# Performance work log

Hardware: AMD Instinct MI355X
Metric: run time of the kernel (lower is better)

## Reference

```python
import jax, jax.numpy as jnp
import numpy as np
from jax import lax

H = 16          # heads
K1, K2 = 3, 3   # kernel_size
LN_EPS = 1e-5


def _ln(x, g, b):
    m = jnp.mean(x, axis=-1, keepdims=True)
    v = jnp.mean(jnp.square(x - m), axis=-1, keepdims=True)
    return (x - m) * lax.rsqrt(v + LN_EPS) * g + b


def _gelu(x):
    return jax.nn.gelu(x, approximate=False)  # torch nn.GELU default (erf)


def setup_inputs() -> dict:
    key = jax.random.key(0)
    B, T, D, Th = 4, 1024, 1024, 256
    C = 2 * D  # context_dim
    ks = jax.random.split(key, 16)

    def w(k, shape):
        fan_in = shape[0]
        return (jax.random.normal(k, shape, jnp.float32) / np.sqrt(fan_in)).astype(jnp.float32)

    inp = {
        'x': jax.random.normal(ks[0], (B, T, D), jnp.float32),
        'historical_data': jax.random.normal(ks[1], (B, Th, D), jnp.float32),
        'Wq': w(ks[2], (D, D)),
        'Wk': w(ks[3], (D, D)),
        'Wv': w(ks[4], (D, D)),
        'hist_W': w(ks[5], (D, C)), 'hist_b': jnp.zeros((C,), jnp.float32),
        'hist_ln_g': jnp.ones((C,), jnp.float32), 'hist_ln_b': jnp.zeros((C,), jnp.float32),
        'ctx_W1': w(ks[6], (C, C // 4)), 'ctx_b1': jnp.zeros((C // 4,), jnp.float32),
        'ctx_W2': w(ks[7], (C // 4, 1)), 'ctx_b2': jnp.zeros((1,), jnp.float32),
        'kg_W1': w(ks[8], (C, D)), 'kg_b1': jnp.zeros((D,), jnp.float32),
        'kg_ln_g': jnp.ones((D,), jnp.float32), 'kg_ln_b': jnp.zeros((D,), jnp.float32),
        'kg_W2': w(ks[9], (D, H * K1 * K2)), 'kg_b2': jnp.zeros((H * K1 * K2,), jnp.float32),
        'proj_W': w(ks[10], (D, D)), 'proj_b': jnp.zeros((D,), jnp.float32),
        'causal_mask': jnp.triu(jnp.ones((T, T), bool), k=1),  # True = masked
    }
    return inp


def reference(x, historical_data, Wq, Wk, Wv, hist_W, hist_b, hist_ln_g, hist_ln_b,
              ctx_W1, ctx_b1, ctx_W2, ctx_b2, kg_W1, kg_b1, kg_ln_g, kg_ln_b,
              kg_W2, kg_b2, proj_W, proj_b, causal_mask):
    B, T, D = x.shape
    hd = D // H
    scale = hd ** -0.5

    # qkv projections (no bias), split heads -> [B, H, T, hd]
    q = (x @ Wq).reshape(B, T, H, hd).transpose(0, 2, 1, 3)
    k = (x @ Wk).reshape(B, T, H, hd).transpose(0, 2, 1, 3)
    v = (x @ Wv).reshape(B, T, H, hd).transpose(0, 2, 1, 3)

    attn = jnp.einsum('bhqd,bhkd->bhqk', q, k) * scale  # [B,H,T,T]

    # --- causal context from history ---
    eh = _gelu(_ln(historical_data @ hist_W + hist_b, hist_ln_g, hist_ln_b))  # [B,Th,C]
    aw = _gelu(eh @ ctx_W1 + ctx_b1) @ ctx_W2 + ctx_b2                        # [B,Th,1]
    aw = jax.nn.softmax(aw, axis=1)
    cc = jnp.sum(eh * aw, axis=1)                                             # [B,C]

    # --- per-(batch,head) 3x3 kernels ---
    kp = _gelu(_ln(cc @ kg_W1 + kg_b1, kg_ln_g, kg_ln_b)) @ kg_W2 + kg_b2     # [B,H*9]
    kernels = jax.nn.softmax(kp.reshape(B, H, K1 * K2), axis=-1)
    kernels = kernels.reshape(B * H, 1, K1, K2)

    # zero masked scores, then mix neighbors via grouped conv2d (cross-correlation)
    mask = causal_mask[None, None]  # [1,1,T,T]
    attn0 = jnp.where(mask, 0.0, attn).reshape(1, B * H, T, T)
    attn = lax.conv_general_dilated(
        attn0, kernels, window_strides=(1, 1),
        padding=((K1 // 2, K1 // 2), (K2 // 2, K2 // 2)),
        feature_group_count=B * H,
        dimension_numbers=('NCHW', 'OIHW', 'NCHW'),
    ).reshape(B, H, T, T)

    attn = jnp.where(mask, -jnp.inf, attn)
    p = jax.nn.softmax(attn, axis=-1)
    out = jnp.einsum('bhqk,bhkd->bhqd', p, v)           # [B,H,T,hd]
    out = out.transpose(0, 2, 1, 3).reshape(B, T, D)
    return out @ proj_W + proj_b
```

## Files before the change

kernel.cpp:

```cpp
#include <hip/hip_runtime.h>
#include <hip/hip_bf16.h>
#include <math.h>

#define DEV static __device__ __forceinline__

typedef __attribute__((ext_vector_type(4))) float f32x4;
typedef __attribute__((ext_vector_type(8))) __bf16 bf16x8;
typedef __attribute__((ext_vector_type(8))) short s16x8;
typedef __attribute__((ext_vector_type(2))) _Float16 h16x2;

DEV float b2f(short v){ unsigned u = ((unsigned)(unsigned short)v) << 16; float f; __builtin_memcpy(&f, &u, 4); return f; }
DEV short f2b(float f){ unsigned u; __builtin_memcpy(&u, &f, 4); unsigned r = (u + 0x7fffu + ((u >> 16) & 1u)) >> 16; return (short)r; }
DEV short f2h(float f){ _Float16 h = (_Float16)f; short s; __builtin_memcpy(&s, &h, 2); return s; }
DEV h16x2 u2h2(unsigned u){ h16x2 h; __builtin_memcpy(&h, &u, 4); return h; }
DEV float gelu_f(float v){ return 0.5f * v * (1.0f + erff(v * 0.70710678118654752f)); }

DEV void gload16(const void* g, void* l) {
  __builtin_amdgcn_global_load_lds((const __attribute__((address_space(1))) unsigned int*)g,
                                   (__attribute__((address_space(3))) unsigned int*)l, 16, 0, 0);
}

DEV void xy_swz(int& bx, int& by, int nx, int ny) {
  int lin = by * nx + bx;
  int q = (nx * ny) >> 3;
  int l2 = (lin & 7) * q + (lin >> 3);
  bx = l2 % nx; by = l2 / nx;
}

__global__ __launch_bounds__(256) void k_cast_all(const float* __restrict__ x, const float* __restrict__ hist,
                                                  short* __restrict__ xb, short* __restrict__ histb,
                                                  short* __restrict__ q, short* __restrict__ kk){
  int bid = blockIdx.x;
  if (bid >= 2560) {
    int idx = (bid - 2560) * 256 + threadIdx.x;
    int bh = idx >> 5, c = idx & 31;
    int which = c >> 3, chunk = c & 7;
    short* base = (which < 2) ? q : kk;
    size_t off = (size_t)bh * 1026 * 64 + ((which & 1) ? (size_t)1025 * 64 : 0) + chunk * 8;
    s16x8 zz = {};
    *(s16x8*)&base[off] = zz;
    return;
  }
  const float* in; short* out; int i;
  if (bid < 2048) { in = x; out = xb; i = (bid * 256 + threadIdx.x) * 8; }
  else            { in = hist; out = histb; i = ((bid - 2048) * 256 + threadIdx.x) * 8; }
  f32x4 a = *(const f32x4*)&in[i];
  f32x4 b = *(const f32x4*)&in[i + 4];
  s16x8 o;
  o[0]=f2b(a[0]); o[1]=f2b(a[1]); o[2]=f2b(a[2]); o[3]=f2b(a[3]);
  o[4]=f2b(b[0]); o[5]=f2b(b[1]); o[6]=f2b(b[2]); o[7]=f2b(b[3]);
  *(s16x8*)&out[i] = o;
}

DEV void tcast_tile(const float* __restrict__ W, short* __restrict__ Wt, int K, int N, int tx, int ty){
  __shared__ float tile[32][33];
  int nb = tx * 32, kb = ty * 32;
  int tid = threadIdx.x;
  int c = tid & 31, r0 = tid >> 5;
  #pragma unroll
  for (int r = r0; r < 32; r += 8) tile[r][c] = W[(size_t)(kb + r) * N + nb + c];
  __syncthreads();
  #pragma unroll
  for (int r = r0; r < 32; r += 8) Wt[(size_t)(nb + r) * K + kb + c] = f2b(tile[c][r]);
}
__global__ __launch_bounds__(256) void k_tcast_all(const float* __restrict__ Wq, const float* __restrict__ Wk,
                                                   const float* __restrict__ Wv, const float* __restrict__ projW,
                                                   const float* __restrict__ histW, const float* __restrict__ ctxW1,
                                                   short* __restrict__ wqkvt, short* __restrict__ wptb,
                                                   short* __restrict__ whtb, short* __restrict__ wc1tb){
  int bid = blockIdx.x;
  const float* W; short* Wt; int K, N, tx, ty;
  if (bid < 4096) {
    int seg = bid >> 10, t = bid & 1023;
    tx = t & 31; ty = t >> 5; K = 1024; N = 1024;
    if      (seg == 0) { W = Wq;    Wt = wqkvt; }
    else if (seg == 1) { W = Wk;    Wt = wqkvt + 1024*1024; }
    else if (seg == 2) { W = Wv;    Wt = wqkvt + 2*1024*1024; }
    else               { W = projW; Wt = wptb; }
  } else if (bid < 6144) {
    int t = bid - 4096; tx = t & 63; ty = t >> 6; K = 1024; N = 2048; W = histW; Wt = whtb;
  } else {
    int t = bid - 6144; tx = t & 15; ty = t >> 4; K = 2048; N = 512; W = ctxW1; Wt = wc1tb;
  }
  tcast_tile(W, Wt, K, N, tx, ty);
}

DEV void gemm_core(const short* __restrict__ A, const short* __restrict__ Bt,
                   int Ks, int lda, int ldb, int m0, int n0,
                   short* lA, short* lB, f32x4 acc[4][4])
{
  const int tid = threadIdx.x;
  const int lane = tid & 63;
  const int w = tid >> 6;
  const int wr = (w >> 1) * 64, wc = (w & 1) * 64;
  const int lr = lane & 15, lk = (lane >> 4) * 8;
  for (int kt = 0; kt < Ks; kt += 64) {
    __syncthreads();
    #pragma unroll
    for (int i = 0; i < 4; ++i) {
      int off = i * 2048 + tid * 8;
      int r = off >> 6, c = off & 63;
      gload16(&A[(size_t)(m0 + r) * lda + kt + c], &lA[off]);
      gload16(&Bt[(size_t)(n0 + r) * ldb + kt + c], &lB[off]);
    }
    __syncthreads();
    #pragma unroll
    for (int kk = 0; kk < 64; kk += 32) {
      bf16x8 af[4], bfr[4];
      #pragma unroll
      for (int mi = 0; mi < 4; ++mi) af[mi] = *(bf16x8*)&lA[(wr + mi*16 + lr)*64 + kk + lk];
      #pragma unroll
      for (int ni = 0; ni < 4; ++ni) bfr[ni] = *(bf16x8*)&lB[(wc + ni*16 + lr)*64 + kk + lk];
      #pragma unroll
      for (int mi = 0; mi < 4; ++mi)
        #pragma unroll
        for (int ni = 0; ni < 4; ++ni)
          acc[mi][ni] = __builtin_amdgcn_mfma_f32_16x16x32_bf16(af[mi], bfr[ni], acc[mi][ni], 0, 0, 0);
    }
  }
}

__global__ __launch_bounds__(256) void k_gemm_f32out(const short* __restrict__ A, const short* __restrict__ Bt,
                                                     float* __restrict__ Cout, const float* __restrict__ bias,
                                                     int N, int lda, int Ks, int mode)
{
  __shared__ __align__(16) short lds[2 * 128 * 64];
  f32x4 acc[4][4] = {};
  int bx = blockIdx.x, by = blockIdx.y;
  xy_swz(bx, by, gridDim.x, gridDim.y);
  int m0 = by * 128, n0 = bx * 128;
  int koff = blockIdx.z * Ks;
  gemm_core(A + koff, Bt + koff, Ks, lda, lda, m0, n0, lds, lds + 128*64, acc);
  Cout += (size_t)blockIdx.z * gridDim.y * 128 * N;
  int lane = threadIdx.x & 63, w = threadIdx.x >> 6;
  int wr = (w>>1)*64, wc = (w&1)*64, lr4 = (lane>>4)*4, lc = lane & 15;
  #pragma unroll
  for (int mi = 0; mi < 4; ++mi)
    #pragma unroll
    for (int ni = 0; ni < 4; ++ni)
      #pragma unroll
      for (int r = 0; r < 4; ++r) {
        int row = m0 + wr + mi*16 + lr4 + r;
        int col = n0 + wc + ni*16 + lc;
        float v = acc[mi][ni][r];
        if (mode != 2) v += bias[col];
        if (mode == 1) v = gelu_f(v);
        Cout[(size_t)row * N + col] = v;
      }
}

__global__ __launch_bounds__(256) void k_gemm_qkv(const short* __restrict__ xb, const short* __restrict__ wqkvt,
                                                  short* __restrict__ q, short* __restrict__ kk, short* __restrict__ vt)
{
  __shared__ __align__(16) short lds[128 * 136];
  f32x4 acc[4][4] = {};
  int bx = blockIdx.x, by = blockIdx.y;
  xy_swz(bx, by, gridDim.x, gridDim.y);
  int m0 = by * 128, n0 = bx * 128;
  gemm_core(xb, wqkvt, 1024, 1024, 1024, m0, n0, lds, lds + 128*64, acc);
  int tid = threadIdx.x, lane = tid & 63, w = tid >> 6;
  int wr = (w>>1)*64, wc = (w&1)*64, lr4 = (lane>>4)*4, lc = lane & 15;
  int bb = m0 >> 10, tm0 = m0 & 1023;
  int s = n0 >> 10, dn0 = n0 & 1023;
  __syncthreads();
  if (s < 2) {
    short* dst = (s == 0) ? q : kk;
    #pragma unroll
    for (int mi = 0; mi < 4; ++mi)
      #pragma unroll
      for (int ni = 0; ni < 4; ++ni)
        #pragma unroll
        for (int r = 0; r < 4; ++r)
          lds[(wr + mi*16 + lr4 + r) * 136 + wc + ni*16 + lc] = f2b(acc[mi][ni][r]);
    __syncthreads();
    #pragma unroll
    for (int it = 0; it < 8; ++it) {
      int idx = it * 256 + tid;
      int row = idx >> 4, ch = (idx & 15) * 8;
      int dfull = dn0 + ch;
      *(s16x8*)&dst[((size_t)(bb*16 + (dfull >> 6)) * 1026 + 1 + tm0 + row) * 64 + (dfull & 63)]
          = *(s16x8*)&lds[row * 136 + ch];
    }
  } else {
    #pragma unroll
    for (int mi = 0; mi < 4; ++mi)
      #pragma unroll
      for (int ni = 0; ni < 4; ++ni)
        #pragma unroll
        for (int r = 0; r < 4; ++r)
          lds[(wc + ni*16 + lc) * 136 + wr + mi*16 + lr4 + r] = f2b(acc[mi][ni][r]);
    __syncthreads();
    #pragma unroll
    for (int it = 0; it < 8; ++it) {
      int idx = it * 256 + tid;
      int nl = idx >> 4, mc = (idx & 15) * 8;
      int dfull = dn0 + nl;
      *(s16x8*)&vt[(((size_t)(bb*16 + (dfull >> 6)) * 64 + (dfull & 63)) << 10) + tm0 + mc]
          = *(s16x8*)&lds[nl * 136 + mc];
    }
  }
}

constexpr int ASTR = 144;

DEV void conv_chunk(const short* sS, int g, int c,
                    const h16x2 wp01[3], const h16x2 wp2z[3], float o[8]) {
  #pragma unroll
  for (int dr = 0; dr < 3; ++dr) {
    int base = (g + dr) * ASTR + 8 + c;
    const unsigned* W = (const unsigned*)&sS[base];
    unsigned U0 = W[0], U1 = W[1], U2 = W[2], U3 = W[3];
    unsigned hm1 = (unsigned short)sS[base - 1];
    unsigned hp8 = (unsigned short)sS[base + 8];
    unsigned P0 = hm1 | (U0 << 16);
    unsigned P2 = (U0 >> 16) | (U1 << 16);
    unsigned P4 = (U1 >> 16) | (U2 << 16);
    unsigned P6 = (U2 >> 16) | (U3 << 16);
    unsigned P8 = (U3 >> 16) | (hp8 << 16);
    unsigned P9 = hp8;
    unsigned pr[10] = {P0, U0, P2, U1, P4, U2, P6, U3, P8, P9};
    h16x2 a = wp01[dr], bz = wp2z[dr];
    #pragma unroll
    for (int t = 0; t < 8; ++t) {
      o[t] = __builtin_amdgcn_fdot2(a,  u2h2(pr[t]),     o[t], false);
      o[t] = __builtin_amdgcn_fdot2(bz, u2h2(pr[t + 2]), o[t], false);
    }
  }
}

__global__ __launch_bounds__(512, 4) void k_attn(const short* __restrict__ q, const short* __restrict__ kkg,
                                                 const short* __restrict__ vt, const float* __restrict__ kern,
                                                 short* __restrict__ O)
{
  __shared__ __align__(16) short lK[2][144 * 64];
  __shared__ __align__(16) short lS[130 * ASTR];
  __shared__ float sInv[128];

  int bh = blockIdx.y, b = bh >> 4, h = bh & 15;
  int qt = (bh >= 32) ? 7 - blockIdx.x : blockIdx.x;
  int m0 = qt * 128;
  int tid = threadIdx.x;
  int w = tid >> 6, lane = tid & 63;
  int lr = lane & 15, lk = (lane >> 4) * 8;

  const short* qp = q   + (size_t)bh * 1026 * 64;
  const short* kp = kkg + (size_t)bh * 1026 * 64;

  h16x2 wp01[3], wp2z[3];
  #pragma unroll
  for (int a = 0; a < 3; ++a) {
    wp01[a][0] = (_Float16)kern[bh * 9 + a * 3 + 0];
    wp01[a][1] = (_Float16)kern[bh * 9 + a * 3 + 1];
    wp2z[a][0] = (_Float16)kern[bh * 9 + a * 3 + 2];
    wp2z[a][1] = (_Float16)0.0f;
  }

  bf16x8 qf0, qf1;
  {
    const short* qrow = &qp[(size_t)(m0 + 1 + w * 16 + lr) * 64];
    qf0 = *(const bf16x8*)&qrow[lk];
    qf1 = *(const bf16x8*)&qrow[32 + lk];
  }
  int hr = -1, hl = 0;
  if (tid < 130) { hr = 0; hl = tid; }
  else if (tid >= 256 && tid < 386) { hr = 129; hl = tid - 256; }

  s16x8 zz = {};
  for (int t = tid; t < 14 * 8; t += 512) {
    *(s16x8*)&lK[0][(130 * 8 + t) * 8] = zz;
    *(s16x8*)&lK[1][(130 * 8 + t) * 8] = zz;
  }
  for (int t = tid; t < 130 * 8; t += 512) {
    int r = t >> 3;
    gload16(&kp[((size_t)r) * 64 + (((t & 7) ^ (r & 7)) << 3)], &lK[0][t * 8]);
  }

  f32x4 pacc[4] = {};
  float psum = 0.0f;
  int g = tid >> 2, qc = tid & 3;
  int cur = 0;

  for (int ct = 0; ct <= qt; ++ct) {
    int n0 = ct * 128;
    __syncthreads();
    if (ct < qt) {
      int n1 = n0 + 128;
      for (int t = tid; t < 130 * 8; t += 512) {
        int r = t >> 3;
        gload16(&kp[((size_t)(n1 + r)) * 64 + (((t & 7) ^ (r & 7)) << 3)], &lK[cur ^ 1][t * 8]);
      }
    }
    const short* lKc = lK[cur];

    int ntmax = (ct == qt) ? (w + 2) : 9;
    int G0 = lk >> 3;
    for (int nt = 0; nt < ntmax; ++nt) {
      int krow = nt * 16 + lr;
      int sw = (krow & 7) << 3;
      bf16x8 bk0 = *(bf16x8*)&lKc[krow * 64 + (( G0      << 3) ^ sw)];
      bf16x8 bk1 = *(bf16x8*)&lKc[krow * 64 + (((G0 + 4) << 3) ^ sw)];
      f32x4 acc = {};
      acc = __builtin_amdgcn_mfma_f32_16x16x32_bf16(qf0, bk0, acc, 0, 0, 0);
      acc = __builtin_amdgcn_mfma_f32_16x16x32_bf16(qf1, bk1, acc, 0, 0, 0);
      int cloc = nt * 16 + lr - 1;
      if (cloc <= 128) {
        #pragma unroll
        for (int r = 0; r < 4; ++r) {
          int rl = w * 16 + (lane >> 4) * 4 + r;
          float v = acc[r] * 0.125f;
          if (n0 + cloc > m0 + rl) v = 0.0f;
          lS[(rl + 1) * ASTR + 8 + cloc] = f2h(v);
        }
      }
    }
    if (hr >= 0) {
      int cloc = hl - 1;
      float s = 0.0f;
      if (n0 + cloc <= m0 - 1 + hr) {
        const short* qrow = &qp[(size_t)(m0 + hr) * 64];
        int krow = cloc + 1;
        int swh = (krow & 7) << 3;
        #pragma unroll
        for (int G = 0; G < 8; ++G) {
          s16x8 qv = *(const s16x8*)&qrow[G * 8];
          s16x8 kv = *(const s16x8*)&lKc[krow * 64 + ((G << 3) ^ swh)];
          #pragma unroll
          for (int j = 0; j < 8; ++j) s += b2f(qv[j]) * b2f(kv[j]);
        }
        s *= 0.125f;
      }
      lS[hr * ASTR + 8 + cloc] = f2h(s);
    }
    __syncthreads();

    s16x8 ps[4];
    #pragma unroll
    for (int j = 0; j < 4; ++j) {
      int c = qc * 8 + j * 32;
      bool live = (ct < qt) || (c <= g);
      float o[8] = {};
      if (live) conv_chunk(lS, g, c, wp01, wp2z, o);
      int glim = (ct == qt) ? g : 127;
      s16x8 po;
      #pragma unroll
      for (int t = 0; t < 8; ++t) {
        float e = (live && (c + t <= glim)) ? __expf(o[t]) : 0.0f;
        psum += e;
        po[t] = f2b(e);
      }
      ps[j] = po;
    }
    __syncthreads();

    #pragma unroll
    for (int j = 0; j < 4; ++j)
      *(s16x8*)&lS[g * ASTR + 8 + qc * 8 + j * 32] = ps[j];
    __syncthreads();

    int kl = 128;
    if (ct == qt) { kl = ((w * 16 + 16 + 31) >> 5) << 5; if (kl > 128) kl = 128; }
    for (int k0 = 0; k0 < kl; k0 += 32) {
      bf16x8 a = *(bf16x8*)&lS[(w * 16 + lr) * ASTR + 8 + k0 + lk];
      #pragma unroll
      for (int dt = 0; dt < 4; ++dt) {
        bf16x8 bv = *(const bf16x8*)&vt[(((size_t)bh * 64 + dt * 16 + lr) << 10) + n0 + k0 + lk];
        pacc[dt] = __builtin_amdgcn_mfma_f32_16x16x32_bf16(a, bv, pacc[dt], 0, 0, 0);
      }
    }
    cur ^= 1;
  }

  psum += __shfl_xor(psum, 1);
  psum += __shfl_xor(psum, 2);
  if (qc == 0) sInv[g] = 1.0f / psum;
  __syncthreads();
  #pragma unroll
  for (int dt = 0; dt < 4; ++dt)
    #pragma unroll
    for (int r = 0; r < 4; ++r) {
      int row = w * 16 + (lane >> 4) * 4 + r;
      float ov = pacc[dt][r] * sInv[row];
      O[((size_t)(b * 1024 + m0 + row) << 10) + h * 64 + dt * 16 + lr] = f2b(ov);
    }
}

__global__ __launch_bounds__(256) void k_ln_gelu2048(const float* __restrict__ x, const float* __restrict__ cb,
                                                     const float* __restrict__ g, const float* __restrict__ be,
                                                     short* __restrict__ out)
{
  __shared__ float red[8];
  int row = blockIdx.x, tid = threadIdx.x;
  const float* xr0 = x + (size_t)row * 2048;
  const float* xr1 = x + (size_t)(1024 + row) * 2048;
  int c0 = tid * 8;
  f32x4 a  = *(const f32x4*)&xr0[c0];
  f32x4 bb = *(const f32x4*)&xr0[c0 + 4];
  f32x4 a1 = *(const f32x4*)&xr1[c0];
  f32x4 b1 = *(const f32x4*)&xr1[c0 + 4];
  f32x4 cb0 = *(const f32x4*)&cb[c0], cb1 = *(const f32x4*)&cb[c0 + 4];
  a += a1 + cb0; bb += b1 + cb1;
  float s = 0, s2 = 0;
  #pragma unroll
  for (int t = 0; t < 4; ++t) { s += a[t] + bb[t]; s2 += a[t]*a[t] + bb[t]*bb[t]; }
  #pragma unroll
  for (int off = 32; off; off >>= 1) { s += __shfl_xor(s, off); s2 += __shfl_xor(s2, off); }
  if ((tid & 63) == 0) { red[tid >> 6] = s; red[4 + (tid >> 6)] = s2; }
  __syncthreads();
  s  = red[0] + red[1] + red[2] + red[3];
  s2 = red[4] + red[5] + red[6] + red[7];
  float mean = s * (1.0f / 2048.0f);
  float var  = s2 * (1.0f / 2048.0f) - mean * mean;
  float inv  = rsqrtf(var + 1e-5f);
  f32x4 g0 = *(const f32x4*)&g[c0],  g1 = *(const f32x4*)&g[c0 + 4];
  f32x4 e0 = *(const f32x4*)&be[c0], e1 = *(const f32x4*)&be[c0 + 4];
  s16x8 o;
  #pragma unroll
  for (int t = 0; t < 4; ++t) {
    o[t]     = f2b(gelu_f((a[t]  - mean) * inv * g0[t] + e0[t]));
    o[t + 4] = f2b(gelu_f((bb[t] - mean) * inv * g1[t] + e1[t]));
  }
  *(s16x8*)&out[(size_t)row * 2048 + c0] = o;
}

__global__ __launch_bounds__(256) void k_red_gelu(const float* __restrict__ p, const float* __restrict__ b1,
                                                  float* __restrict__ out)
{
  int i = (blockIdx.x * 256 + threadIdx.x) * 4;
  f32x4 s = *(const f32x4*)&p[i];
  #pragma unroll
  for (int z = 1; z < 4; ++z) s += *(const f32x4*)&p[(size_t)z * 524288 + i];
  f32x4 bv = *(const f32x4*)&b1[i & 511];
  f32x4 o;
  #pragma unroll
  for (int t = 0; t < 4; ++t) o[t] = gelu_f(s[t] + bv[t]);
  *(f32x4*)&out[i] = o;
}

__global__ __launch_bounds__(256) void k_aw_logit(const float* __restrict__ t, const float* __restrict__ w2,
                                                  const float* __restrict__ b2, float* __restrict__ logit)
{
  int row = blockIdx.x * 4 + (threadIdx.x >> 6);
  int lane = threadIdx.x & 63;
  float s = 0;
  for (int c = lane; c < 512; c += 64) s += t[(size_t)row * 512 + c] * w2[c];
  #pragma unroll
  for (int off = 32; off; off >>= 1) s += __shfl_xor(s, off);
  if (lane == 0) logit[row] = s + b2[0];
}

__global__ __launch_bounds__(256) void k_softmax_cc(const float* __restrict__ logit, const short* __restrict__ ehb,
                                                    float* __restrict__ cc)
{
  __shared__ float sw[256];
  __shared__ float red[8];
  int b = blockIdx.y, ch = blockIdx.x, tid = threadIdx.x;
  float v = logit[b * 256 + tid];
  float m = v;
  #pragma unroll
  for (int off = 32; off; off >>= 1) m = fmaxf(m, __shfl_xor(m, off));
  if ((tid & 63) == 0) red[tid >> 6] = m;
  __syncthreads();
  float M = fmaxf(fmaxf(red[0], red[1]), fmaxf(red[2], red[3]));
  float e = __expf(v - M);
  float s = e;
  #pragma unroll
  for (int off = 32; off; off >>= 1) s += __shfl_xor(s, off);
  if ((tid & 63) == 0) red[4 + (tid >> 6)] = s;
  __syncthreads();
  float invS = 1.0f / (red[4] + red[5] + red[6] + red[7]);
  sw[tid] = e * invS;
  __syncthreads();
  int c = ch * 256 + tid;
  float a = 0;
  for (int t = 0; t < 256; ++t) a += sw[t] * b2f(ehb[(((size_t)(b * 256 + t)) << 11) + c]);
  cc[(b << 11) + c] = a;
}

__global__ __launch_bounds__(256) void k_kg1p(const float* __restrict__ cc, const float* __restrict__ W1,
                                              float* __restrict__ part)
{
  int d = blockIdx.x * 256 + threadIdx.x;
  int kc = blockIdx.y;
  float s0 = 0, s1 = 0, s2 = 0, s3 = 0;
  for (int k = kc * 64; k < kc * 64 + 64; ++k) {
    float w = W1[(size_t)k * 1024 + d];
    s0 += cc[k] * w; s1 += cc[2048 + k] * w; s2 += cc[4096 + k] * w; s3 += cc[6144 + k] * w;
  }
  part[(size_t)(kc * 4 + 0) * 1024 + d] = s0;
  part[(size_t)(kc * 4 + 1) * 1024 + d] = s1;
  part[(size_t)(kc * 4 + 2) * 1024 + d] = s2;
  part[(size_t)(kc * 4 + 3) * 1024 + d] = s3;
}

__global__ __launch_bounds__(256) void k_kg_mid(const float* __restrict__ part, const float* __restrict__ b1,
                                                const float* __restrict__ g, const float* __restrict__ be,
                                                short* __restrict__ kgh)
{
  __shared__ float red[8];
  int b = blockIdx.x, tid = threadIdx.x;
  float v[4]; float s = 0, s2 = 0;
  #pragma unroll
  for (int qi = 0; qi < 4; ++qi) {
    int d = tid + qi * 256;
    float acc = b1[d];
    for (int kc = 0; kc < 32; ++kc) acc += part[(size_t)(kc * 4 + b) * 1024 + d];
    v[qi] = acc; s += acc; s2 += acc * acc;
  }
  #pragma unroll
  for (int off = 32; off; off >>= 1) { s += __shfl_xor(s, off); s2 += __shfl_xor(s2, off); }
  if ((tid & 63) == 0) { red[tid >> 6] = s; red[4 + (tid >> 6)] = s2; }
  __syncthreads();
  s  = red[0] + red[1] + red[2] + red[3];
  s2 = red[4] + red[5] + red[6] + red[7];
  float mean = s * (1.0f / 1024.0f);
  float var  = s2 * (1.0f / 1024.0f) - mean * mean;
  float inv  = rsqrtf(var + 1e-5f);
  #pragma unroll
  for (int qi = 0; qi < 4; ++qi) {
    int d = tid + qi * 256;
    kgh[b * 1024 + d] = f2b(gelu_f((v[qi] - mean) * inv * g[d] + be[d]));
  }
}

__global__ __launch_bounds__(64) void k_kp2(const short* __restrict__ kgh, const float* __restrict__ W2,
                                            const float* __restrict__ b2, float* __restrict__ kern)
{
  int h = blockIdx.x, b = blockIdx.y, lane = threadIdx.x;
  float kg[16];
  #pragma unroll
  for (int m = 0; m < 16; ++m) kg[m] = b2f(kgh[b * 1024 + lane + m * 64]);
  float dj[9];
  #pragma unroll
  for (int j = 0; j < 9; ++j) {
    float s = 0;
    #pragma unroll
    for (int m = 0; m < 16; ++m) s += kg[m] * W2[(size_t)(lane + m * 64) * 144 + h * 9 + j];
    #pragma unroll
    for (int off = 32; off; off >>= 1) s += __shfl_xor(s, off);
    dj[j] = s + b2[h * 9 + j];
  }
  if (lane == 0) {
    float m = dj[0];
    #pragma unroll
    for (int j = 1; j < 9; ++j) m = fmaxf(m, dj[j]);
    float e[9], s = 0;
    #pragma unroll
    for (int j = 0; j < 9; ++j) { e[j] = __expf(dj[j] - m); s += e[j]; }
    float inv = 1.0f / s;
    #pragma unroll
    for (int j = 0; j < 9; ++j) kern[(b * 16 + h) * 9 + j] = e[j] * inv;
  }
}

__global__ void k_fail(float* out){ out[threadIdx.x] = 1.0e9f; }

extern "C" void kernel_launch(void* const* d_in, const int* in_sizes, int n_in,
                              void* d_out, int out_size, void* d_ws, size_t ws_size,
                              hipStream_t stream) {
  (void)in_sizes; (void)n_in; (void)out_size;
  const float* x       = (const float*)d_in[0];
  const float* hist    = (const float*)d_in[1];
  const float* Wq      = (const float*)d_in[2];
  const float* Wk      = (const float*)d_in[3];
  const float* Wv      = (const float*)d_in[4];
  const float* hist_W  = (const float*)d_in[5];
  const float* hist_b  = (const float*)d_in[6];
  const float* hln_g   = (const float*)d_in[7];
  const float* hln_b   = (const float*)d_in[8];
  const float* ctx_W1  = (const float*)d_in[9];
  const float* ctx_b1  = (const float*)d_in[10];
  const float* ctx_W2  = (const float*)d_in[11];
  const float* ctx_b2  = (const float*)d_in[12];
  const float* kg_W1   = (const float*)d_in[13];
  const float* kg_b1   = (const float*)d_in[14];
  const float* kln_g   = (const float*)d_in[15];
  const float* kln_b   = (const float*)d_in[16];
  const float* kg_W2   = (const float*)d_in[17];
  const float* kg_b2   = (const float*)d_in[18];
  const float* proj_W  = (const float*)d_in[19];
  const float* proj_b  = (const float*)d_in[20];
  float* outp = (float*)d_out;

  char* wsb = (char*)d_ws;
  size_t off = 0;
  auto nxt = [&](size_t bytes) { void* p = wsb + off; off += (bytes + 255) & ~(size_t)255; return p; };

  short* xb     = (short*)nxt((size_t)4096*1024*2);
  short* wqkvt  = (short*)nxt((size_t)3*1024*1024*2);
  short* qb     = (short*)nxt((size_t)64*1026*64*2);
  short* kb     = (short*)nxt((size_t)64*1026*64*2);
  short* vtb    = (short*)nxt((size_t)64*64*1024*2);
  short* Ob     = (short*)nxt((size_t)4096*1024*2);
  short* histb  = (short*)nxt((size_t)1024*1024*2);
  short* whtb   = (short*)nxt((size_t)2048*1024*2);
  float* ehpreP = (float*)nxt((size_t)2*1024*2048*4);
  short* ehb    = (short*)nxt((size_t)1024*2048*2);
  short* wc1tb  = (short*)nxt((size_t)512*2048*2);
  float* ctxP   = (float*)nxt((size_t)4*1024*512*4);
  float* tbuf   = (float*)nxt((size_t)1024*512*4);
  float* logit  = (float*)nxt((size_t)1024*4);
  float* ccb    = (float*)nxt((size_t)4*2048*4);
  float* kgpart = (float*)nxt((size_t)128*1024*4);
  short* kghb   = (short*)nxt((size_t)4*1024*2);
  float* kernb  = (float*)nxt((size_t)64*9*4);
  short* wptb   = (short*)nxt((size_t)1024*1024*2);

  if (ws_size < off) { k_fail<<<1, 64, 0, stream>>>(outp); return; }

  k_cast_all<<<2568, 256, 0, stream>>>(x, hist, xb, histb, qb, kb);
  k_tcast_all<<<7168, 256, 0, stream>>>(Wq, Wk, Wv, proj_W, hist_W, ctx_W1, wqkvt, wptb, whtb, wc1tb);

  k_gemm_f32out<<<dim3(16, 8, 2), 256, 0, stream>>>(histb, whtb, ehpreP, nullptr, 2048, 1024, 512, 2);
  k_ln_gelu2048<<<1024, 256, 0, stream>>>(ehpreP, hist_b, hln_g, hln_b, ehb);
  k_gemm_f32out<<<dim3(4, 8, 4), 256, 0, stream>>>(ehb, wc1tb, ctxP, nullptr, 512, 2048, 512, 2);
  k_red_gelu<<<512, 256, 0, stream>>>(ctxP, ctx_b1, tbuf);
  k_aw_logit<<<256, 256, 0, stream>>>(tbuf, ctx_W2, ctx_b2, logit);
  k_softmax_cc<<<dim3(8, 4), 256, 0, stream>>>(logit, ehb, ccb);
  k_kg1p<<<dim3(4, 32), 256, 0, stream>>>(ccb, kg_W1, kgpart);
  k_kg_mid<<<4, 256, 0, stream>>>(kgpart, kg_b1, kln_g, kln_b, kghb);
  k_kp2<<<dim3(16, 4), 64, 0, stream>>>(kghb, kg_W2, kg_b2, kernb);

  k_gemm_qkv<<<dim3(24, 32), 256, 0, stream>>>(xb, wqkvt, qb, kb, vtb);
  k_attn<<<dim3(8, 64), 512, 0, stream>>>(qb, kb, vtb, kernb, Ob);
  k_gemm_f32out<<<dim3(8, 32, 1), 256, 0, stream>>>(Ob, wptb, outp, proj_b, 1024, 1024, 1024, 0);
}
```

Before: 280.9 us.

## Map conv output directly to MFMA A-operand layout, drop P writeback to LDS

```diff
diff --git a/kernel.cpp b/kernel.cpp
--- a/kernel.cpp
+++ b/kernel.cpp
@@ -201,7 +201,7 @@
   }
 }
 
-constexpr int ASTR = 144;
+constexpr int ASTR = 148;
 
 DEV void conv_chunk(const short* sS, int g, int c,
                     const h16x2 wp01[3], const h16x2 wp2z[3], float o[8]) {
@@ -234,14 +234,14 @@
 {
   __shared__ __align__(16) short lK[2][144 * 64];
   __shared__ __align__(16) short lS[130 * ASTR];
-  __shared__ float sInv[128];
 
   int bh = blockIdx.y, b = bh >> 4, h = bh & 15;
   int qt = (bh >= 32) ? 7 - blockIdx.x : blockIdx.x;
   int m0 = qt * 128;
   int tid = threadIdx.x;
   int w = tid >> 6, lane = tid & 63;
-  int lr = lane & 15, lk = (lane >> 4) * 8;
+  int lr = lane & 15, hi = lane >> 4;
+  int lk = hi * 8;
 
   const short* qp = q   + (size_t)bh * 1026 * 64;
   const short* kp = kkg + (size_t)bh * 1026 * 64;
@@ -257,13 +257,16 @@
 
   bf16x8 qf0, qf1;
   {
-    const short* qrow = &qp[(size_t)(m0 + 1 + w * 16 + lr) * 64];
+    const short* qrow = &qp[(size_t)(m0 + w * 16 + lr) * 64];
     qf0 = *(const bf16x8*)&qrow[lk];
     qf1 = *(const bf16x8*)&qrow[32 + lk];
   }
-  int hr = -1, hl = 0;
-  if (tid < 130) { hr = 0; hl = tid; }
-  else if (tid >= 256 && tid < 386) { hr = 129; hl = tid - 256; }
+  bf16x8 qe0, qe1;
+  {
+    const short* qrow = &qp[(size_t)(m0 + 114 + lr) * 64];
+    qe0 = *(const bf16x8*)&qrow[lk];
+    qe1 = *(const bf16x8*)&qrow[32 + lk];
+  }
 
   s16x8 zz = {};
   for (int t = tid; t < 14 * 8; t += 512) {
@@ -277,7 +280,6 @@
 
   f32x4 pacc[4] = {};
   float psum = 0.0f;
-  int g = tid >> 2, qc = tid & 3;
   int cur = 0;
 
   for (int ct = 0; ct <= qt; ++ct) {
@@ -293,50 +295,54 @@
     const short* lKc = lK[cur];
 
     int ntmax = (ct == qt) ? (w + 2) : 9;
-    int G0 = lk >> 3;
     for (int nt = 0; nt < ntmax; ++nt) {
       int krow = nt * 16 + lr;
       int sw = (krow & 7) << 3;
-      bf16x8 bk0 = *(bf16x8*)&lKc[krow * 64 + (( G0      << 3) ^ sw)];
-      bf16x8 bk1 = *(bf16x8*)&lKc[krow * 64 + (((G0 + 4) << 3) ^ sw)];
+      bf16x8 bk0 = *(bf16x8*)&lKc[krow * 64 + (( hi      << 3) ^ sw)];
+      bf16x8 bk1 = *(bf16x8*)&lKc[krow * 64 + (((hi + 4) << 3) ^ sw)];
       f32x4 acc = {};
       acc = __builtin_amdgcn_mfma_f32_16x16x32_bf16(qf0, bk0, acc, 0, 0, 0);
       acc = __builtin_amdgcn_mfma_f32_16x16x32_bf16(qf1, bk1, acc, 0, 0, 0);
-      int cloc = nt * 16 + lr - 1;
+      int cloc = krow - 1;
       if (cloc <= 128) {
         #pragma unroll
         for (int r = 0; r < 4; ++r) {
-          int rl = w * 16 + (lane >> 4) * 4 + r;
+          int rl = w * 16 + hi * 4 + r;
           float v = acc[r] * 0.125f;
-          if (n0 + cloc > m0 + rl) v = 0.0f;
-          lS[(rl + 1) * ASTR + 8 + cloc] = f2h(v);
+          if (n0 + cloc > m0 - 1 + rl) v = 0.0f;
+          lS[rl * ASTR + 8 + cloc] = f2h(v);
         }
       }
     }
-    if (hr >= 0) {
-      int cloc = hl - 1;
-      float s = 0.0f;
-      if (n0 + cloc <= m0 - 1 + hr) {
-        const short* qrow = &qp[(size_t)(m0 + hr) * 64];
-        int krow = cloc + 1;
-        int swh = (krow & 7) << 3;
+    #pragma unroll
+    for (int e = 0; e < 2; ++e) {
+      if (e == 1 && w != 0) break;
+      int nt = (e == 0) ? w : 8;
+      int krow = nt * 16 + lr;
+      int sw = (krow & 7) << 3;
+      bf16x8 bk0 = *(bf16x8*)&lKc[krow * 64 + (( hi      << 3) ^ sw)];
+      bf16x8 bk1 = *(bf16x8*)&lKc[krow * 64 + (((hi + 4) << 3) ^ sw)];
+      f32x4 acc = {};
+      acc = __builtin_amdgcn_mfma_f32_16x16x32_bf16(qe0, bk0, acc, 0, 0, 0);
+      acc = __builtin_amdgcn_mfma_f32_16x16x32_bf16(qe1, bk1, acc, 0, 0, 0);
+      int cloc = krow - 1;
+      if (hi == 3 && cloc <= 128) {
         #pragma unroll
-        for (int G = 0; G < 8; ++G) {
-          s16x8 qv = *(const s16x8*)&qrow[G * 8];
-          s16x8 kv = *(const s16x8*)&lKc[krow * 64 + ((G << 3) ^ swh)];
-          #pragma unroll
-          for (int j = 0; j < 8; ++j) s += b2f(qv[j]) * b2f(kv[j]);
+        for (int r = 2; r < 4; ++r) {
+          int rowt = 12 + r;
+          float v = acc[r] * 0.125f;
+          if (n0 + cloc > m0 + 113 + rowt) v = 0.0f;
+          lS[(114 + rowt) * ASTR + 8 + cloc] = f2h(v);
         }
-        s *= 0.125f;
       }
-      lS[hr * ASTR + 8 + cloc] = f2h(s);
     }
     __syncthreads();
 
-    s16x8 ps[4];
+    int g = w * 16 + lr;
+    s16x8 pa[4];
     #pragma unroll
     for (int j = 0; j < 4; ++j) {
-      int c = qc * 8 + j * 32;
+      int c = hi * 8 + 32 * j;
       bool live = (ct < qt) || (c <= g);
       float o[8] = {};
       if (live) conv_chunk(lS, g, c, wp01, wp2z, o);
@@ -348,40 +354,38 @@
         psum += e;
         po[t] = f2b(e);
       }
-      ps[j] = po;
-    }
-    __syncthreads();
-
-    #pragma unroll
-    for (int j = 0; j < 4; ++j)
-      *(s16x8*)&lS[g * ASTR + 8 + qc * 8 + j * 32] = ps[j];
-    __syncthreads();
+      pa[j] = po;
+    }
 
     int kl = 128;
     if (ct == qt) { kl = ((w * 16 + 16 + 31) >> 5) << 5; if (kl > 128) kl = 128; }
-    for (int k0 = 0; k0 < kl; k0 += 32) {
-      bf16x8 a = *(bf16x8*)&lS[(w * 16 + lr) * ASTR + 8 + k0 + lk];
-      #pragma unroll
-      for (int dt = 0; dt < 4; ++dt) {
-        bf16x8 bv = *(const bf16x8*)&vt[(((size_t)bh * 64 + dt * 16 + lr) << 10) + n0 + k0 + lk];
-        pacc[dt] = __builtin_amdgcn_mfma_f32_16x16x32_bf16(a, bv, pacc[dt], 0, 0, 0);
+    #pragma unroll
+    for (int j = 0; j < 4; ++j) {
+      if (j * 32 < kl) {
+        bf16x8 af;
+        __builtin_memcpy(&af, &pa[j], 16);
+        #pragma unroll
+        for (int dt = 0; dt < 4; ++dt) {
+          bf16x8 bv = *(const bf16x8*)&vt[(((size_t)bh * 64 + dt * 16 + lr) << 10) + n0 + j * 32 + lk];
+          pacc[dt] = __builtin_amdgcn_mfma_f32_16x16x32_bf16(af, bv, pacc[dt], 0, 0, 0);
+        }
       }
     }
     cur ^= 1;
   }
 
-  psum += __shfl_xor(psum, 1);
-  psum += __shfl_xor(psum, 2);
-  if (qc == 0) sInv[g] = 1.0f / psum;
-  __syncthreads();
-  #pragma unroll
-  for (int dt = 0; dt < 4; ++dt)
-    #pragma unroll
-    for (int r = 0; r < 4; ++r) {
-      int row = w * 16 + (lane >> 4) * 4 + r;
-      float ov = pacc[dt][r] * sInv[row];
+  psum += __shfl_xor(psum, 16);
+  psum += __shfl_xor(psum, 32);
+  #pragma unroll
+  for (int r = 0; r < 4; ++r) {
+    float sInvR = 1.0f / __shfl(psum, hi * 4 + r, 64);
+    int row = w * 16 + hi * 4 + r;
+    #pragma unroll
+    for (int dt = 0; dt < 4; ++dt) {
+      float ov = pacc[dt][r] * sInvR;
       O[((size_t)(b * 1024 + m0 + row) << 10) + h * 64 + dt * 16 + lr] = f2b(ov);
     }
+  }
 }
 
 __global__ __launch_bounds__(256) void k_ln_gelu2048(const float* __restrict__ x, const float* __restrict__ cb,
```

After: 263.1 us. 6.4% less time.
